# Kernel optimization log

Hardware: AMD Instinct MI355X
Metric: run time of the kernel (lower is better)

Reference implementation:

```python
import jax, jax.numpy as jnp
import numpy as np

BS, TS, NE, ED = 32, 64, 64, 128
AE = 256          # attn_embed_dim
NH = 4            # attn heads
HD = AE // NH     # head dim
RH = 256          # rnn_hidden_dim
NA = 8            # n_agents
NACT = 64         # n_actions
NEG = -1e10


def setup_inputs() -> dict:
    key = jax.random.key(0)
    ks = iter(jax.random.split(key, 64))
    def g(shape, s=0.05):
        return jax.random.normal(next(ks), shape, dtype=jnp.float32) * s
    inp = dict(
        entities=g((BS, TS, NE, ED), 1.0),
        obs_mask=jax.random.randint(next(ks), (BS, TS, NE, NE), 0, 2, dtype=jnp.int32),
        entity_mask=jax.random.randint(next(ks), (BS, TS, NE), 0, 2, dtype=jnp.int32),
        hidden_q=g((BS, NA, RH), 1.0),
        hidden_pi=g((BS, NA, RH), 1.0),
    )
    for p in ('q', 'p'):
        inp[f'{p}_fc1_w'] = g((AE, ED)); inp[f'{p}_fc1_b'] = g((AE,))
        inp[f'{p}_fc2_w'] = g((RH, AE)); inp[f'{p}_fc2_b'] = g((RH,))
        inp[f'{p}_gru_wih'] = g((3 * RH, RH)); inp[f'{p}_gru_whh'] = g((3 * RH, RH))
        inp[f'{p}_gru_bih'] = g((3 * RH,)); inp[f'{p}_gru_bhh'] = g((3 * RH,))
        inp[f'{p}_fcq_w'] = g((NACT, RH)); inp[f'{p}_fcq_b'] = g((NACT,))
        inp[f'{p}_fcpi_w'] = g((NACT, RH)); inp[f'{p}_fcpi_b'] = g((NACT,))
    inp['q_attn_in_w'] = g((3 * AE, AE))
    inp['q_attn_out_w'] = g((AE, AE)); inp['q_attn_out_b'] = g((AE,))
    return inp


def _attention(x1, pre_mask, in_w, out_w, out_b):
    # x1: [B, NE, AE]; pre_mask: [B, NA, NE] (1 = masked)
    qkv = x1 @ in_w.T                                   # [B, NE, 3*AE]
    q, k, v = jnp.split(qkv, 3, axis=-1)
    q = q[:, :NA].reshape(-1, NA, NH, HD).transpose(0, 2, 1, 3)   # [B,H,NA,HD]
    k = k.reshape(-1, NE, NH, HD).transpose(0, 2, 1, 3)           # [B,H,NE,HD]
    v = v.reshape(-1, NE, NH, HD).transpose(0, 2, 1, 3)
    logits = jnp.einsum('bhqd,bhkd->bhqk', q, k) / jnp.sqrt(jnp.float32(HD))
    m = (pre_mask[:, None, :, :] != 0)                  # [B,1,NA,NE]
    dead = jnp.all(m, axis=-1, keepdims=True)           # fully-masked rows -> NaN fix
    logits = jnp.where(m, -jnp.inf, logits)
    logits = jnp.where(dead, 0.0, logits)
    w = jax.nn.softmax(logits, axis=-1)
    w = jnp.where(dead, 0.0, w)                         # torch: masked_fill(NaN, 0)
    out = jnp.einsum('bhqk,bhkd->bhqd', w, v)
    out = out.transpose(0, 2, 1, 3).reshape(-1, NA, AE)
    return out @ out_w.T + out_b


def _gru_scan(x3, h0, wih, whh, bih, bhh):
    # x3: [BS, TS, NA, RH]; h0: [BS*NA, RH]
    xt = x3.transpose(1, 0, 2, 3).reshape(TS, BS * NA, RH)
    def step(h, x):
        gi = x @ wih.T + bih
        gh = h @ whh.T + bhh
        ir, iz, inn = jnp.split(gi, 3, axis=-1)
        hr, hz, hn = jnp.split(gh, 3, axis=-1)
        r = jax.nn.sigmoid(ir + hr)
        z = jax.nn.sigmoid(iz + hz)
        n = jnp.tanh(inn + r * hn)
        h_new = (1.0 - z) * n + z * h
        return h_new, h_new
    _, hs = jax.lax.scan(step, h0, xt)
    return hs.reshape(TS, BS, NA, RH).transpose(1, 0, 2, 3)       # [BS,TS,NA,RH]


def _module(entities, obs_mask, entity_mask, hidden, use_attn,
            fc1_w, fc1_b, fc2_w, fc2_b, gru_wih, gru_whh, gru_bih, gru_bhh,
            fcq_w, fcq_b, fcpi_w, fcpi_b, attn=None):
    B = BS * TS
    e = entities.reshape(B, NE, ED)
    om = obs_mask.reshape(B, NE, NE)
    em = entity_mask.reshape(B, NE)
    agent_mask = em[:, :NA]                              # [B, NA]
    x1 = jax.nn.relu(e @ fc1_w.T + fc1_b)                # [B, NE, AE]
    if use_attn:
        in_w, out_w, out_b = attn
        x2 = _attention(x1, om[:, :NA], in_w, out_w, out_b)
        x2 = jnp.where(agent_mask[:, :, None] != 0, 0.0, x2)   # post_mask
    else:
        x2 = x1[:, :NA]
    x3 = jax.nn.relu(x2 @ fc2_w.T + fc2_b).reshape(BS, TS, NA, RH)
    hs = _gru_scan(x3, hidden.reshape(-1, RH), gru_wih, gru_whh, gru_bih, gru_bhh)
    oq = hs @ fcq_w.T + fcq_b
    opi = hs @ fcpi_w.T + fcpi_b
    am = (agent_mask.reshape(BS, TS, NA, 1) != 0)
    oq = jnp.where(am, 0.0, oq)
    opi = jnp.where(am, NEG, opi)
    return oq, opi, hs


def reference(entities, obs_mask, entity_mask, hidden_q, hidden_pi,
              q_fc1_w, q_fc1_b, q_attn_in_w, q_attn_out_w, q_attn_out_b,
              q_fc2_w, q_fc2_b, q_gru_wih, q_gru_whh, q_gru_bih, q_gru_bhh,
              q_fcq_w, q_fcq_b, q_fcpi_w, q_fcpi_b,
              p_fc1_w, p_fc1_b, p_fc2_w, p_fc2_b,
              p_gru_wih, p_gru_whh, p_gru_bih, p_gru_bhh,
              p_fcq_w, p_fcq_b, p_fcpi_w, p_fcpi_b):
    q, pi, h_q = _module(entities, obs_mask, entity_mask, hidden_q, True,
                         q_fc1_w, q_fc1_b, q_fc2_w, q_fc2_b,
                         q_gru_wih, q_gru_whh, q_gru_bih, q_gru_bhh,
                         q_fcq_w, q_fcq_b, q_fcpi_w, q_fcpi_b,
                         attn=(q_attn_in_w, q_attn_out_w, q_attn_out_b))
    _, pi_avg, h_pi = _module(entities, obs_mask, entity_mask, hidden_pi, False,
                              p_fc1_w, p_fc1_b, p_fc2_w, p_fc2_b,
                              p_gru_wih, p_gru_whh, p_gru_bih, p_gru_bhh,
                              p_fcq_w, p_fcq_b, p_fcpi_w, p_fcpi_b)
    return (q, pi, pi_avg, h_q, h_pi)
```

## Files before the change

### kernel.cpp

```cpp
#include <hip/hip_runtime.h>

typedef unsigned short ushort_t;
typedef __attribute__((ext_vector_type(4))) float f32x4;
typedef __attribute__((ext_vector_type(8))) short s16x8;
typedef __attribute__((ext_vector_type(4))) short s16x4;

#define MFMA16(a, b, c) __builtin_amdgcn_mfma_f32_16x16x32_bf16((a), (b), (c), 0, 0, 0)

__device__ __forceinline__ float us2f(unsigned short u) {
  union { unsigned int i; float f; } v; v.i = ((unsigned int)u) << 16; return v.f;
}
__device__ __forceinline__ unsigned short f2us(float f) {
  union { float f; unsigned int i; } v; v.f = f;
  unsigned int x = v.i;
  return (unsigned short)((x + 0x7FFFu + ((x >> 16) & 1u)) >> 16);
}
__device__ __forceinline__ s16x8 ld8f(const float* p) {
  f32x4 a = *reinterpret_cast<const f32x4*>(p);
  f32x4 b = *reinterpret_cast<const f32x4*>(p + 4);
  s16x8 r;
  r[0] = (short)f2us(a[0]); r[1] = (short)f2us(a[1]);
  r[2] = (short)f2us(a[2]); r[3] = (short)f2us(a[3]);
  r[4] = (short)f2us(b[0]); r[5] = (short)f2us(b[1]);
  r[6] = (short)f2us(b[2]); r[7] = (short)f2us(b[3]);
  return r;
}
__device__ __forceinline__ float sigm(float x) { return 1.0f / (1.0f + __expf(-x)); }
__device__ __forceinline__ float tanh_f(float x) {
  float e = __expf(-2.0f * fabsf(x));
  float t = (1.0f - e) / (1.0f + e);
  return x < 0.0f ? -t : t;
}

__global__ __launch_bounds__(256) void conv_k(
    const float* __restrict__ s0, const float* __restrict__ s1,
    const float* __restrict__ s2, const float* __restrict__ s3,
    ushort_t* __restrict__ d) {
  int i = blockIdx.x * 256 + threadIdx.x;
  if (i >= 155648) return;
  long e = (long)i * 4;
  const float* s; long off;
  if (e < 196608) { s = s0; off = e; }
  else if (e < 393216) { s = s1; off = e - 196608; }
  else if (e < 425984) { s = s2; off = e - 393216; }
  else { s = s3; off = e - 425984; }
  f32x4 v = *reinterpret_cast<const f32x4*>(s + off);
  s16x4 r;
  r[0] = (short)f2us(v[0]); r[1] = (short)f2us(v[1]);
  r[2] = (short)f2us(v[2]); r[3] = (short)f2us(v[3]);
  *reinterpret_cast<s16x4*>(d + e) = r;
}

template <int BN, int EPI, int ROWSEL, int RELU, int AF32, int OF32, int GIT>
__global__ __launch_bounds__(256) void gemm_k(
    const void* __restrict__ A_, const float* __restrict__ W,
    const float* __restrict__ bias, const int* __restrict__ em,
    void* __restrict__ out_, int M, int N, int K) {
  constexpr int NF = (BN == 128) ? 4 : 2;
  const float* Af = (const float*)A_;
  const ushort_t* Ab = (const ushort_t*)A_;
  float* outf = (float*)out_;
  ushort_t* outb = (ushort_t*)out_;
  __shared__ ushort_t As[128 * 40];
  __shared__ ushort_t Ws[BN * 40];
  const int tid = threadIdx.x;
  const int lane = tid & 63;
  const int wid = tid >> 6;
  const int wm = wid & 1, wn = wid >> 1;
  const int m0 = blockIdx.x * 128;
  const int n0 = blockIdx.y * BN;
  const int fr = lane & 15;
  const int kb = (lane >> 4) * 8;

  f32x4 acc[4][NF];
#pragma unroll
  for (int i = 0; i < 4; i++)
#pragma unroll
    for (int j = 0; j < NF; j++) acc[i][j] = (f32x4){0.f, 0.f, 0.f, 0.f};

  for (int k0 = 0; k0 < K; k0 += 32) {
    __syncthreads();
    for (int c = tid; c < 512; c += 256) {
      int row = c >> 2, kc = (c & 3) * 8;
      int gr = m0 + row;
      long ar = ROWSEL ? ((long)(gr >> 3) * 64 + (gr & 7)) : (long)gr;
      s16x8 vv;
      if (AF32) vv = ld8f(&Af[ar * (long)K + k0 + kc]);
      else vv = *reinterpret_cast<const s16x8*>(&Ab[ar * (long)K + k0 + kc]);
      *reinterpret_cast<s16x8*>(&As[row * 40 + kc]) = vv;
    }
    for (int c = tid; c < BN * 4; c += 256) {
      int row = c >> 2, kc = (c & 3) * 8;
      *reinterpret_cast<s16x8*>(&Ws[row * 40 + kc]) =
          ld8f(&W[(long)(n0 + row) * K + k0 + kc]);
    }
    __syncthreads();
    s16x8 af[4], wf[NF];
#pragma unroll
    for (int mi = 0; mi < 4; mi++)
      af[mi] = *reinterpret_cast<const s16x8*>(&As[(wm * 64 + mi * 16 + fr) * 40 + kb]);
#pragma unroll
    for (int ni = 0; ni < NF; ni++)
      wf[ni] = *reinterpret_cast<const s16x8*>(&Ws[(wn * (BN / 2) + ni * 16 + fr) * 40 + kb]);
#pragma unroll
    for (int mi = 0; mi < 4; mi++)
#pragma unroll
      for (int ni = 0; ni < NF; ni++) acc[mi][ni] = MFMA16(af[mi], wf[ni], acc[mi][ni]);
  }

  const int rb = (lane >> 4) * 4;
#pragma unroll
  for (int ni = 0; ni < NF; ni++) {
    int col = n0 + wn * (BN / 2) + ni * 16 + fr;
    float bv = bias[col];
#pragma unroll
    for (int mi = 0; mi < 4; mi++) {
#pragma unroll
      for (int rr = 0; rr < 4; rr++) {
        int row = m0 + wm * 64 + mi * 16 + rb + rr;
        float v = acc[mi][ni][rr] + bv;
        if (RELU) v = fmaxf(v, 0.0f);
        if (EPI == 2 || EPI == 3) {
          if (em[(long)(row >> 3) * 64 + (row & 7)] != 0) v = (EPI == 2) ? 0.0f : -1.0e10f;
        }
        if (GIT) {
          int t = (row >> 3) & 63, bs = row >> 9, na = row & 7;
          int chain = bs * 8 + na;
          int g = col >> 8, cw = col & 255;
          outb[(((long)t * 3 + g) * 16 + (chain >> 4)) * 4096 + cw * 16 + (chain & 15)] =
              f2us(v);
        } else if (OF32) {
          outf[(long)row * N + col] = v;
        } else {
          outb[(long)row * N + col] = f2us(v);
        }
      }
    }
  }
}

__global__ __launch_bounds__(512) void attn_k(
    const float* __restrict__ ent, const int* __restrict__ obs,
    const ushort_t* __restrict__ fc1w, const float* __restrict__ fc1b,
    const ushort_t* __restrict__ inw, ushort_t* __restrict__ attn_out) {
  __shared__ ushort_t x1s[64 * 264];
  __shared__ ushort_t ks[64 * 264];
  __shared__ ushort_t vs[64 * 264];
  __shared__ ushort_t wbuf[256 * 40];
  __shared__ ushort_t es[64 * 136];
  __shared__ float qs[8 * 256];
  __shared__ float lg[32 * 64];
  __shared__ int oms[512];

  const long b = blockIdx.x;
  const int tid = threadIdx.x;
  const int lane = tid & 63, wid = tid >> 6;
  const int mf = wid & 3, nh = wid >> 2;
  const int fr = lane & 15, kb = (lane >> 4) * 8, rb = (lane >> 4) * 4;

  oms[tid] = obs[b * 4096 + tid];
  for (int c = tid; c < 1024; c += 512) {
    int row = c >> 4, kc = (c & 15) * 8;
    *reinterpret_cast<s16x8*>(&es[row * 136 + kc]) =
        ld8f(&ent[b * 8192 + row * 128 + kc]);
  }
  __syncthreads();

  {
    f32x4 a1[8];
#pragma unroll
    for (int i = 0; i < 8; i++) a1[i] = (f32x4){0.f, 0.f, 0.f, 0.f};
    for (int k0 = 0; k0 < 128; k0 += 32) {
      __syncthreads();
      for (int c = tid; c < 1024; c += 512) {
        int row = c >> 2, kc = (c & 3) * 8;
        *reinterpret_cast<s16x8*>(&wbuf[row * 40 + kc]) =
            *reinterpret_cast<const s16x8*>(&fc1w[row * 128 + k0 + kc]);
      }
      __syncthreads();
      s16x8 af = *reinterpret_cast<const s16x8*>(&es[(mf * 16 + fr) * 136 + k0 + kb]);
#pragma unroll
      for (int ni = 0; ni < 8; ni++) {
        s16x8 wf = *reinterpret_cast<const s16x8*>(&wbuf[(nh * 128 + ni * 16 + fr) * 40 + kb]);
        a1[ni] = MFMA16(af, wf, a1[ni]);
      }
    }
#pragma unroll
    for (int ni = 0; ni < 8; ni++) {
      int col = nh * 128 + ni * 16 + fr;
      float bv = fc1b[col];
#pragma unroll
      for (int rr = 0; rr < 4; rr++) {
        int row = mf * 16 + rb + rr;
        x1s[row * 264 + col] = f2us(fmaxf(a1[ni][rr] + bv, 0.0f));
      }
    }
  }
  {
    f32x4 a2[8];
#pragma unroll
    for (int i = 0; i < 8; i++) a2[i] = (f32x4){0.f, 0.f, 0.f, 0.f};
    for (int k0 = 0; k0 < 256; k0 += 32) {
      __syncthreads();
      for (int c = tid; c < 1024; c += 512) {
        int row = c >> 2, kc = (c & 3) * 8;
        *reinterpret_cast<s16x8*>(&wbuf[row * 40 + kc]) =
            *reinterpret_cast<const s16x8*>(&inw[65536 + row * 256 + k0 + kc]);
      }
      __syncthreads();
      s16x8 af = *reinterpret_cast<const s16x8*>(&x1s[(mf * 16 + fr) * 264 + k0 + kb]);
#pragma unroll
      for (int ni = 0; ni < 8; ni++) {
        s16x8 wf = *reinterpret_cast<const s16x8*>(&wbuf[(nh * 128 + ni * 16 + fr) * 40 + kb]);
        a2[ni] = MFMA16(af, wf, a2[ni]);
      }
    }
#pragma unroll
    for (int ni = 0; ni < 8; ni++) {
      int col = nh * 128 + ni * 16 + fr;
#pragma unroll
      for (int rr = 0; rr < 4; rr++) ks[(mf * 16 + rb + rr) * 264 + col] = f2us(a2[ni][rr]);
    }
  }
  {
    f32x4 a3[8];
#pragma unroll
    for (int i = 0; i < 8; i++) a3[i] = (f32x4){0.f, 0.f, 0.f, 0.f};
    for (int k0 = 0; k0 < 256; k0 += 32) {
      __syncthreads();
      for (int c = tid; c < 1024; c += 512) {
        int row = c >> 2, kc = (c & 3) * 8;
        *reinterpret_cast<s16x8*>(&wbuf[row * 40 + kc]) =
            *reinterpret_cast<const s16x8*>(&inw[131072 + row * 256 + k0 + kc]);
      }
      __syncthreads();
      s16x8 af = *reinterpret_cast<const s16x8*>(&x1s[(mf * 16 + fr) * 264 + k0 + kb]);
#pragma unroll
      for (int ni = 0; ni < 8; ni++) {
        s16x8 wf = *reinterpret_cast<const s16x8*>(&wbuf[(nh * 128 + ni * 16 + fr) * 40 + kb]);
        a3[ni] = MFMA16(af, wf, a3[ni]);
      }
    }
#pragma unroll
    for (int ni = 0; ni < 8; ni++) {
      int col = nh * 128 + ni * 16 + fr;
#pragma unroll
      for (int rr = 0; rr < 4; rr++) vs[(mf * 16 + rb + rr) * 264 + col] = f2us(a3[ni][rr]);
    }
  }
  {
    f32x4 aq[2];
    aq[0] = (f32x4){0.f, 0.f, 0.f, 0.f};
    aq[1] = (f32x4){0.f, 0.f, 0.f, 0.f};
    for (int k0 = 0; k0 < 256; k0 += 32) {
      __syncthreads();
      for (int c = tid; c < 1024; c += 512) {
        int row = c >> 2, kc = (c & 3) * 8;
        *reinterpret_cast<s16x8*>(&wbuf[row * 40 + kc]) =
            *reinterpret_cast<const s16x8*>(&inw[row * 256 + k0 + kc]);
      }
      __syncthreads();
      s16x8 af = *reinterpret_cast<const s16x8*>(&x1s[fr * 264 + k0 + kb]);
#pragma unroll
      for (int i = 0; i < 2; i++) {
        int nf2 = wid * 2 + i;
        s16x8 wf = *reinterpret_cast<const s16x8*>(&wbuf[(nf2 * 16 + fr) * 40 + kb]);
        aq[i] = MFMA16(af, wf, aq[i]);
      }
    }
#pragma unroll
    for (int i = 0; i < 2; i++) {
#pragma unroll
      for (int rr = 0; rr < 4; rr++) {
        int row = rb + rr;
        if (row < 8) qs[row * 256 + (wid * 2 + i) * 16 + fr] = aq[i][rr] * 0.125f;
      }
    }
  }
  __syncthreads();

  for (int i = 0; i < 4; i++) {
    int idx = tid + 512 * i;
    int a = idx >> 8, h = (idx >> 6) & 3, e = idx & 63;
    const float* qrow = &qs[a * 256 + h * 64];
    const ushort_t* krow = &ks[e * 264 + h * 64];
    float s = 0.0f;
    for (int d = 0; d < 64; d++) s += qrow[d] * us2f(krow[d]);
    lg[(a * 4 + h) * 64 + e] = (oms[a * 64 + e] != 0) ? -1.0e30f : s;
  }
  __syncthreads();
  if (tid < 32) {
    int a = tid >> 2;
    float* row = &lg[tid * 64];
    bool dead = true;
    for (int e = 0; e < 64; e++)
      if (oms[a * 64 + e] == 0) { dead = false; break; }
    if (dead) {
      for (int e = 0; e < 64; e++) row[e] = 0.0f;
    } else {
      float mx = -1.0e30f;
      for (int e = 0; e < 64; e++) mx = fmaxf(mx, row[e]);
      float sum = 0.0f;
      for (int e = 0; e < 64; e++) { float ex = __expf(row[e] - mx); row[e] = ex; sum += ex; }
      float inv = 1.0f / sum;
      for (int e = 0; e < 64; e++) row[e] *= inv;
    }
  }
  __syncthreads();
  for (int i = 0; i < 4; i++) {
    int idx = tid + 512 * i;
    int a = idx >> 8, d = idx & 255, h = d >> 6;
    const float* wrow = &lg[(a * 4 + h) * 64];
    float s = 0.0f;
    for (int e = 0; e < 64; e++) s += wrow[e] * us2f(vs[e * 264 + d]);
    attn_out[((long)b * 8 + a) * 256 + d] = f2us(s);
  }
}

__global__ __launch_bounds__(1024) void gru3_k(
    const ushort_t* __restrict__ giT_q, const ushort_t* __restrict__ giT_p,
    const ushort_t* __restrict__ whhb_q, const ushort_t* __restrict__ whhb_p,
    const float* __restrict__ bhh_q, const float* __restrict__ bhh_p,
    const float* __restrict__ h0_q, const float* __restrict__ h0_p,
    float* __restrict__ hs_q, float* __restrict__ hs_p) {
  __shared__ ushort_t nw[256 * 256];
  __shared__ ushort_t hls[16 * 260];
  const int bid = blockIdx.x;
  const int mdl = bid >> 4, cg = bid & 15;
  const ushort_t* giT = mdl ? giT_p : giT_q;
  const ushort_t* whh = mdl ? whhb_p : whhb_q;
  const float* bhh = mdl ? bhh_p : bhh_q;
  const float* h0 = mdl ? h0_p : h0_q;
  float* hs = mdl ? hs_p : hs_q;

  const int tid = threadIdx.x;
  const int lane = tid & 63, w = tid >> 6;
  const int fr = lane & 15, kb = (lane >> 4) * 8, rb = (lane >> 4) * 4;
  const int c0 = w * 16;
  const int col = c0 + fr;

  s16x8 wrz[2][8];
#pragma unroll
  for (int g = 0; g < 2; g++)
#pragma unroll
    for (int ks = 0; ks < 8; ks++)
      wrz[g][ks] = *reinterpret_cast<const s16x8*>(
          &whh[(g * 256 + col) * 256 + ks * 32 + kb]);

  char* nwb = (char*)nw;
  for (int c = tid; c < 8192; c += 1024) {
    int row = c >> 5, kc = (c & 31) * 8;
    *reinterpret_cast<s16x8*>(nwb + row * 512 + ((kc * 2) ^ ((row & 7) << 4))) =
        *reinterpret_cast<const s16x8*>(&whh[(512 + row) * 256 + kc]);
  }

  float h[4], bh[3];
#pragma unroll
  for (int rr = 0; rr < 4; rr++) h[rr] = h0[(cg * 16 + rb + rr) * 256 + col];
#pragma unroll
  for (int g = 0; g < 3; g++) bh[g] = bhh[g * 256 + col];

  long hsb[4];
#pragma unroll
  for (int rr = 0; rr < 4; rr++) {
    int chain = cg * 16 + rb + rr;
    hsb[rr] = ((long)((chain >> 3) * 64) * 8 + (chain & 7)) * 256 + col;
  }

  for (int t = 0; t < 64; t++) {
    s16x4 gv[3];
#pragma unroll
    for (int g = 0; g < 3; g++)
      gv[g] = *reinterpret_cast<const s16x4*>(
          &giT[(((long)t * 3 + g) * 16 + cg) * 4096 + col * 16 + rb]);
#pragma unroll
    for (int rr = 0; rr < 4; rr++) hls[(rb + rr) * 260 + col] = f2us(h[rr]);
    __syncthreads();
    f32x4 acc[3];
#pragma unroll
    for (int i = 0; i < 3; i++) acc[i] = (f32x4){0.f, 0.f, 0.f, 0.f};
#pragma unroll
    for (int ks = 0; ks < 8; ks++) {
      s16x8 a = *reinterpret_cast<const s16x8*>(&hls[fr * 260 + ks * 32 + kb]);
      acc[0] = MFMA16(a, wrz[0][ks], acc[0]);
      acc[1] = MFMA16(a, wrz[1][ks], acc[1]);
      s16x8 bn = *reinterpret_cast<const s16x8*>(
          nwb + col * 512 + (((ks * 32 + kb) * 2) ^ ((col & 7) << 4)));
      acc[2] = MFMA16(a, bn, acc[2]);
    }
    __syncthreads();
#pragma unroll
    for (int rr = 0; rr < 4; rr++) {
      float r_ = sigm(us2f((unsigned short)gv[0][rr]) + acc[0][rr] + bh[0]);
      float z_ = sigm(us2f((unsigned short)gv[1][rr]) + acc[1][rr] + bh[1]);
      float n_ = tanh_f(us2f((unsigned short)gv[2][rr]) + r_ * (acc[2][rr] + bh[2]));
      float hn = (1.0f - z_) * n_ + z_ * h[rr];
      h[rr] = hn;
      hs[hsb[rr] + (long)t * 2048] = hn;
    }
  }
}

extern "C" void kernel_launch(void* const* d_in, const int* in_sizes, int n_in,
                              void* d_out, int out_size, void* d_ws, size_t ws_size,
                              hipStream_t stream) {
  (void)in_sizes; (void)n_in; (void)out_size; (void)ws_size;

  const float* entities = (const float*)d_in[0];
  const int* obs = (const int*)d_in[1];
  const int* em = (const int*)d_in[2];
  const float* hidq = (const float*)d_in[3];
  const float* hidp = (const float*)d_in[4];
  const float* q_fc1_w = (const float*)d_in[5];
  const float* q_fc1_b = (const float*)d_in[6];
  const float* q_fc2_w = (const float*)d_in[7];
  const float* q_fc2_b = (const float*)d_in[8];
  const float* q_wih = (const float*)d_in[9];
  const float* q_whh = (const float*)d_in[10];
  const float* q_bih = (const float*)d_in[11];
  const float* q_bhh = (const float*)d_in[12];
  const float* q_fcq_w = (const float*)d_in[13];
  const float* q_fcq_b = (const float*)d_in[14];
  const float* q_fcpi_w = (const float*)d_in[15];
  const float* q_fcpi_b = (const float*)d_in[16];
  const float* p_fc1_w = (const float*)d_in[17];
  const float* p_fc1_b = (const float*)d_in[18];
  const float* p_fc2_w = (const float*)d_in[19];
  const float* p_fc2_b = (const float*)d_in[20];
  const float* p_wih = (const float*)d_in[21];
  const float* p_whh = (const float*)d_in[22];
  const float* p_bih = (const float*)d_in[23];
  const float* p_bhh = (const float*)d_in[24];
  const float* p_fcpi_w = (const float*)d_in[27];
  const float* p_fcpi_b = (const float*)d_in[28];
  const float* inw = (const float*)d_in[29];
  const float* outw = (const float*)d_in[30];
  const float* outb = (const float*)d_in[31];

  ushort_t* ws = (ushort_t*)d_ws;
  ushort_t* R0 = ws;
  ushort_t* R1 = ws + 4194304l;
  ushort_t* giq = ws + 8388608l;
  ushort_t* gip = ws + 20971520l;
  ushort_t* wcv = ws + 33554432l;
  ushort_t* wbq = wcv;
  ushort_t* wbp = wcv + 196608l;
  ushort_t* wf1 = wcv + 393216l;
  ushort_t* win = wcv + 425984l;

  float* out = (float*)d_out;
  float* o_q = out;
  float* o_pi = out + 1048576l;
  float* o_piA = out + 2097152l;
  float* o_hq = out + 3145728l;
  float* o_hp = out + 7340032l;

  conv_k<<<608, 256, 0, stream>>>(q_whh, p_whh, q_fc1_w, inw, wcv);
  attn_k<<<2048, 512, 0, stream>>>(entities, obs, wf1, q_fc1_b, win, R0);
  gemm_k<128, 2, 0, 0, 0, 0, 0><<<dim3(128, 2), 256, 0, stream>>>(R0, outw, outb, em, R1, 16384, 256, 256);
  gemm_k<128, 0, 0, 1, 0, 0, 0><<<dim3(128, 2), 256, 0, stream>>>(R1, q_fc2_w, q_fc2_b, em, R0, 16384, 256, 256);
  gemm_k<128, 0, 0, 0, 0, 0, 1><<<dim3(128, 6), 256, 0, stream>>>(R0, q_wih, q_bih, em, giq, 16384, 768, 256);
  gemm_k<128, 0, 1, 1, 1, 0, 0><<<dim3(128, 2), 256, 0, stream>>>(entities, p_fc1_w, p_fc1_b, em, R1, 16384, 256, 128);
  gemm_k<128, 0, 0, 1, 0, 0, 0><<<dim3(128, 2), 256, 0, stream>>>(R1, p_fc2_w, p_fc2_b, em, R0, 16384, 256, 256);
  gemm_k<128, 0, 0, 0, 0, 0, 1><<<dim3(128, 6), 256, 0, stream>>>(R0, p_wih, p_bih, em, gip, 16384, 768, 256);
  gru3_k<<<32, 1024, 0, stream>>>(giq, gip, wbq, wbp, q_bhh, p_bhh, hidq, hidp,
                                  o_hq, o_hp);
  gemm_k<64, 2, 0, 0, 1, 1, 0><<<dim3(128, 1), 256, 0, stream>>>(o_hq, q_fcq_w, q_fcq_b, em, o_q, 16384, 64, 256);
  gemm_k<64, 3, 0, 0, 1, 1, 0><<<dim3(128, 1), 256, 0, stream>>>(o_hq, q_fcpi_w, q_fcpi_b, em, o_pi, 16384, 64, 256);
  gemm_k<64, 3, 0, 0, 1, 1, 0><<<dim3(128, 1), 256, 0, stream>>>(o_hp, p_fcpi_w, p_fcpi_b, em, o_piA, 16384, 64, 256);
}
```

Before: 556.9 us.

## Split attention into batched fc1/QKV GEMMs plus MFMA-based attention kernel

The monolithic per-batch attention kernel, which recomputed fc1 and the Q/K/V projections with weights streamed through shared memory for every block, is replaced by large tiled GEMMs for fc1 and the fused QKV projection, followed by a lighter attention kernel. That kernel computes logits with MFMA, runs a parallel shuffle-based softmax and vectorises the weighted V sum. Work is chunked by workspace size, and the weight conversion kernel shrinks. It adds intermediate global traffic for x1 and K/V, plus chunked launches when the workspace is small.

After: 714.6 us. 28.3% more time.

```diff
diff --git a/kernel.cpp b/kernel.cpp
--- a/kernel.cpp
+++ b/kernel.cpp
@@ -34,16 +34,13 @@
 
 __global__ __launch_bounds__(256) void conv_k(
     const float* __restrict__ s0, const float* __restrict__ s1,
-    const float* __restrict__ s2, const float* __restrict__ s3,
     ushort_t* __restrict__ d) {
   int i = blockIdx.x * 256 + threadIdx.x;
-  if (i >= 155648) return;
+  if (i >= 98304) return;
   long e = (long)i * 4;
   const float* s; long off;
   if (e < 196608) { s = s0; off = e; }
-  else if (e < 393216) { s = s1; off = e - 196608; }
-  else if (e < 425984) { s = s2; off = e - 393216; }
-  else { s = s3; off = e - 425984; }
+  else { s = s1; off = e - 196608; }
   f32x4 v = *reinterpret_cast<const f32x4*>(s + off);
   s16x4 r;
   r[0] = (short)f2us(v[0]); r[1] = (short)f2us(v[1]);
@@ -51,11 +48,13 @@
   *reinterpret_cast<s16x4*>(d + e) = r;
 }
 
-template <int BN, int EPI, int ROWSEL, int RELU, int AF32, int OF32, int GIT>
+template <int BN, int EPI, int ROWSEL, int RELU, int AF32, int OF32, int GIT,
+          int QKV, int HB>
 __global__ __launch_bounds__(256) void gemm_k(
     const void* __restrict__ A_, const float* __restrict__ W,
     const float* __restrict__ bias, const int* __restrict__ em,
-    void* __restrict__ out_, int M, int N, int K) {
+    void* __restrict__ out_, ushort_t* __restrict__ qout, long row0,
+    int M, int N, int K) {
   constexpr int NF = (BN == 128) ? 4 : 2;
   const float* Af = (const float*)A_;
   const ushort_t* Ab = (const ushort_t*)A_;
@@ -112,7 +111,7 @@
 #pragma unroll
   for (int ni = 0; ni < NF; ni++) {
     int col = n0 + wn * (BN / 2) + ni * 16 + fr;
-    float bv = bias[col];
+    float bv = HB ? bias[col] : 0.0f;
 #pragma unroll
     for (int mi = 0; mi < 4; mi++) {
 #pragma unroll
@@ -123,7 +122,15 @@
         if (EPI == 2 || EPI == 3) {
           if (em[(long)(row >> 3) * 64 + (row & 7)] != 0) v = (EPI == 2) ? 0.0f : -1.0e10f;
         }
-        if (GIT) {
+        if (QKV) {
+          long grow = row0 + row;
+          int e = (int)(grow & 63);
+          if (col < 256) {
+            if (e < 8) qout[((grow >> 6) * 8 + e) * 256 + col] = f2us(v * 0.125f);
+          } else {
+            outb[(long)row * 512 + (col - 256)] = f2us(v);
+          }
+        } else if (GIT) {
           int t = (row >> 3) & 63, bs = row >> 9, na = row & 7;
           int chain = bs * 8 + na;
           int g = col >> 8, cw = col & 255;
@@ -139,181 +146,105 @@
   }
 }
 
-__global__ __launch_bounds__(512) void attn_k(
-    const float* __restrict__ ent, const int* __restrict__ obs,
-    const ushort_t* __restrict__ fc1w, const float* __restrict__ fc1b,
-    const ushort_t* __restrict__ inw, ushort_t* __restrict__ attn_out) {
-  __shared__ ushort_t x1s[64 * 264];
+__global__ __launch_bounds__(512) void attn2_k(
+    const ushort_t* __restrict__ kv, const ushort_t* __restrict__ qbuf,
+    const int* __restrict__ obs, ushort_t* __restrict__ attn_out, int b0) {
+  __shared__ ushort_t qs[16 * 264];
   __shared__ ushort_t ks[64 * 264];
   __shared__ ushort_t vs[64 * 264];
-  __shared__ ushort_t wbuf[256 * 40];
-  __shared__ ushort_t es[64 * 136];
-  __shared__ float qs[8 * 256];
-  __shared__ float lg[32 * 64];
+  __shared__ float lg[32 * 66];
   __shared__ int oms[512];
 
-  const long b = blockIdx.x;
+  const int b_loc = blockIdx.x;
+  const long b = b0 + b_loc;
   const int tid = threadIdx.x;
-  const int lane = tid & 63, wid = tid >> 6;
-  const int mf = wid & 3, nh = wid >> 2;
+  const int lane = tid & 63;
+  const int w = tid >> 6;
   const int fr = lane & 15, kb = (lane >> 4) * 8, rb = (lane >> 4) * 4;
 
   oms[tid] = obs[b * 4096 + tid];
-  for (int c = tid; c < 1024; c += 512) {
-    int row = c >> 4, kc = (c & 15) * 8;
-    *reinterpret_cast<s16x8*>(&es[row * 136 + kc]) =
-        ld8f(&ent[b * 8192 + row * 128 + kc]);
+  {
+    int row = tid >> 5, cc = (tid & 31) * 8;
+    if (tid < 256) {
+      *reinterpret_cast<s16x8*>(&qs[row * 264 + cc]) =
+          *reinterpret_cast<const s16x8*>(&qbuf[(b * 8 + row) * 256 + cc]);
+    } else {
+      *reinterpret_cast<s16x8*>(&qs[row * 264 + cc]) = (s16x8){0,0,0,0,0,0,0,0};
+    }
+  }
+  for (int i = 0; i < 4; i++) {
+    int e = i * 16 + (tid >> 5);
+    int cc = (tid & 31) * 8;
+    const ushort_t* src = &kv[((long)(b_loc * 64 + e)) * 512];
+    *reinterpret_cast<s16x8*>(&ks[e * 264 + cc]) =
+        *reinterpret_cast<const s16x8*>(&src[cc]);
+    *reinterpret_cast<s16x8*>(&vs[e * 264 + cc]) =
+        *reinterpret_cast<const s16x8*>(&src[256 + cc]);
   }
   __syncthreads();
 
   {
-    f32x4 a1[8];
-#pragma unroll
-    for (int i = 0; i < 8; i++) a1[i] = (f32x4){0.f, 0.f, 0.f, 0.f};
-    for (int k0 = 0; k0 < 128; k0 += 32) {
-      __syncthreads();
-      for (int c = tid; c < 1024; c += 512) {
-        int row = c >> 2, kc = (c & 3) * 8;
-        *reinterpret_cast<s16x8*>(&wbuf[row * 40 + kc]) =
-            *reinterpret_cast<const s16x8*>(&fc1w[row * 128 + k0 + kc]);
+    const int h = w >> 1, np = w & 1;
+    f32x4 lacc[2];
+    lacc[0] = (f32x4){0.f, 0.f, 0.f, 0.f};
+    lacc[1] = (f32x4){0.f, 0.f, 0.f, 0.f};
+#pragma unroll
+    for (int k0 = 0; k0 < 64; k0 += 32) {
+      s16x8 af = *reinterpret_cast<const s16x8*>(&qs[fr * 264 + h * 64 + k0 + kb]);
+#pragma unroll
+      for (int j = 0; j < 2; j++) {
+        int e0 = (np * 2 + j) * 16;
+        s16x8 bf = *reinterpret_cast<const s16x8*>(&ks[(e0 + fr) * 264 + h * 64 + k0 + kb]);
+        lacc[j] = MFMA16(af, bf, lacc[j]);
       }
-      __syncthreads();
-      s16x8 af = *reinterpret_cast<const s16x8*>(&es[(mf * 16 + fr) * 136 + k0 + kb]);
-#pragma unroll
-      for (int ni = 0; ni < 8; ni++) {
-        s16x8 wf = *reinterpret_cast<const s16x8*>(&wbuf[(nh * 128 + ni * 16 + fr) * 40 + kb]);
-        a1[ni] = MFMA16(af, wf, a1[ni]);
+    }
+#pragma unroll
+    for (int j = 0; j < 2; j++) {
+      int e = (np * 2 + j) * 16 + fr;
+#pragma unroll
+      for (int rr = 0; rr < 4; rr++) {
+        int a = rb + rr;
+        if (a < 8)
+          lg[(a * 4 + h) * 66 + e] = (oms[a * 64 + e] != 0) ? -1.0e30f : lacc[j][rr];
       }
     }
-#pragma unroll
-    for (int ni = 0; ni < 8; ni++) {
-      int col = nh * 128 + ni * 16 + fr;
-      float bv = fc1b[col];
-#pragma unroll
-      for (int rr = 0; rr < 4; rr++) {
-        int row = mf * 16 + rb + rr;
-        x1s[row * 264 + col] = f2us(fmaxf(a1[ni][rr] + bv, 0.0f));
-      }
-    }
-  }
+  }
+  __syncthreads();
+
   {
-    f32x4 a2[8];
-#pragma unroll
-    for (int i = 0; i < 8; i++) a2[i] = (f32x4){0.f, 0.f, 0.f, 0.f};
-    for (int k0 = 0; k0 < 256; k0 += 32) {
-      __syncthreads();
-      for (int c = tid; c < 1024; c += 512) {
-        int row = c >> 2, kc = (c & 3) * 8;
-        *reinterpret_cast<s16x8*>(&wbuf[row * 40 + kc]) =
-            *reinterpret_cast<const s16x8*>(&inw[65536 + row * 256 + k0 + kc]);
-      }
-      __syncthreads();
-      s16x8 af = *reinterpret_cast<const s16x8*>(&x1s[(mf * 16 + fr) * 264 + k0 + kb]);
-#pragma unroll
-      for (int ni = 0; ni < 8; ni++) {
-        s16x8 wf = *reinterpret_cast<const s16x8*>(&wbuf[(nh * 128 + ni * 16 + fr) * 40 + kb]);
-        a2[ni] = MFMA16(af, wf, a2[ni]);
-      }
-    }
-#pragma unroll
-    for (int ni = 0; ni < 8; ni++) {
-      int col = nh * 128 + ni * 16 + fr;
-#pragma unroll
-      for (int rr = 0; rr < 4; rr++) ks[(mf * 16 + rb + rr) * 264 + col] = f2us(a2[ni][rr]);
-    }
-  }
+    int ri = tid >> 4, sub = tid & 15;
+    float v4[4];
+#pragma unroll
+    for (int j = 0; j < 4; j++) v4[j] = lg[ri * 66 + sub * 4 + j];
+    float m = fmaxf(fmaxf(v4[0], v4[1]), fmaxf(v4[2], v4[3]));
+#pragma unroll
+    for (int d = 1; d < 16; d <<= 1) m = fmaxf(m, __shfl_xor(m, d));
+    bool dead = (m < -5.0e29f);
+    float s = 0.0f;
+#pragma unroll
+    for (int j = 0; j < 4; j++) { v4[j] = __expf(v4[j] - m); s += v4[j]; }
+#pragma unroll
+    for (int d = 1; d < 16; d <<= 1) s += __shfl_xor(s, d);
+    float inv = dead ? 0.0f : (1.0f / s);
+#pragma unroll
+    for (int j = 0; j < 4; j++) lg[ri * 66 + sub * 4 + j] = v4[j] * inv;
+  }
+  __syncthreads();
+
   {
-    f32x4 a3[8];
-#pragma unroll
-    for (int i = 0; i < 8; i++) a3[i] = (f32x4){0.f, 0.f, 0.f, 0.f};
-    for (int k0 = 0; k0 < 256; k0 += 32) {
-      __syncthreads();
-      for (int c = tid; c < 1024; c += 512) {
-        int row = c >> 2, kc = (c & 3) * 8;
-        *reinterpret_cast<s16x8*>(&wbuf[row * 40 + kc]) =
-            *reinterpret_cast<const s16x8*>(&inw[131072 + row * 256 + k0 + kc]);
-      }
-      __syncthreads();
-      s16x8 af = *reinterpret_cast<const s16x8*>(&x1s[(mf * 16 + fr) * 264 + k0 + kb]);
-#pragma unroll
-      for (int ni = 0; ni < 8; ni++) {
-        s16x8 wf = *reinterpret_cast<const s16x8*>(&wbuf[(nh * 128 + ni * 16 + fr) * 40 + kb]);
-        a3[ni] = MFMA16(af, wf, a3[ni]);
-      }
-    }
-#pragma unroll
-    for (int ni = 0; ni < 8; ni++) {
-      int col = nh * 128 + ni * 16 + fr;
-#pragma unroll
-      for (int rr = 0; rr < 4; rr++) vs[(mf * 16 + rb + rr) * 264 + col] = f2us(a3[ni][rr]);
-    }
-  }
-  {
-    f32x4 aq[2];
-    aq[0] = (f32x4){0.f, 0.f, 0.f, 0.f};
-    aq[1] = (f32x4){0.f, 0.f, 0.f, 0.f};
-    for (int k0 = 0; k0 < 256; k0 += 32) {
-      __syncthreads();
-      for (int c = tid; c < 1024; c += 512) {
-        int row = c >> 2, kc = (c & 3) * 8;
-        *reinterpret_cast<s16x8*>(&wbuf[row * 40 + kc]) =
-            *reinterpret_cast<const s16x8*>(&inw[row * 256 + k0 + kc]);
-      }
-      __syncthreads();
-      s16x8 af = *reinterpret_cast<const s16x8*>(&x1s[fr * 264 + k0 + kb]);
-#pragma unroll
-      for (int i = 0; i < 2; i++) {
-        int nf2 = wid * 2 + i;
-        s16x8 wf = *reinterpret_cast<const s16x8*>(&wbuf[(nf2 * 16 + fr) * 40 + kb]);
-        aq[i] = MFMA16(af, wf, aq[i]);
-      }
-    }
-#pragma unroll
-    for (int i = 0; i < 2; i++) {
-#pragma unroll
-      for (int rr = 0; rr < 4; rr++) {
-        int row = rb + rr;
-        if (row < 8) qs[row * 256 + (wid * 2 + i) * 16 + fr] = aq[i][rr] * 0.125f;
-      }
-    }
-  }
-  __syncthreads();
-
-  for (int i = 0; i < 4; i++) {
-    int idx = tid + 512 * i;
-    int a = idx >> 8, h = (idx >> 6) & 3, e = idx & 63;
-    const float* qrow = &qs[a * 256 + h * 64];
-    const ushort_t* krow = &ks[e * 264 + h * 64];
-    float s = 0.0f;
-    for (int d = 0; d < 64; d++) s += qrow[d] * us2f(krow[d]);
-    lg[(a * 4 + h) * 64 + e] = (oms[a * 64 + e] != 0) ? -1.0e30f : s;
-  }
-  __syncthreads();
-  if (tid < 32) {
-    int a = tid >> 2;
-    float* row = &lg[tid * 64];
-    bool dead = true;
-    for (int e = 0; e < 64; e++)
-      if (oms[a * 64 + e] == 0) { dead = false; break; }
-    if (dead) {
-      for (int e = 0; e < 64; e++) row[e] = 0.0f;
-    } else {
-      float mx = -1.0e30f;
-      for (int e = 0; e < 64; e++) mx = fmaxf(mx, row[e]);
-      float sum = 0.0f;
-      for (int e = 0; e < 64; e++) { float ex = __expf(row[e] - mx); row[e] = ex; sum += ex; }
-      float inv = 1.0f / sum;
-      for (int e = 0; e < 64; e++) row[e] *= inv;
-    }
-  }
-  __syncthreads();
-  for (int i = 0; i < 4; i++) {
-    int idx = tid + 512 * i;
-    int a = idx >> 8, d = idx & 255, h = d >> 6;
-    const float* wrow = &lg[(a * 4 + h) * 64];
-    float s = 0.0f;
-    for (int e = 0; e < 64; e++) s += wrow[e] * us2f(vs[e * 264 + d]);
-    attn_out[((long)b * 8 + a) * 256 + d] = f2us(s);
+    int a = tid >> 6, d0 = (tid & 63) * 4, h = d0 >> 6;
+    const float* wrow = &lg[(a * 4 + h) * 66];
+    float facc[4] = {0.f, 0.f, 0.f, 0.f};
+    for (int e = 0; e < 64; e++) {
+      float wv = wrow[e];
+      s16x4 vv = *reinterpret_cast<const s16x4*>(&vs[e * 264 + d0]);
+#pragma unroll
+      for (int j = 0; j < 4; j++) facc[j] += wv * us2f((unsigned short)vv[j]);
+    }
+    s16x4 r;
+#pragma unroll
+    for (int j = 0; j < 4; j++) r[j] = (short)f2us(facc[j]);
+    *reinterpret_cast<s16x4*>(&attn_out[(b * 8 + a) * 256 + d0]) = r;
   }
 }
 
@@ -336,8 +267,7 @@
   const int tid = threadIdx.x;
   const int lane = tid & 63, w = tid >> 6;
   const int fr = lane & 15, kb = (lane >> 4) * 8, rb = (lane >> 4) * 4;
-  const int c0 = w * 16;
-  const int col = c0 + fr;
+  const int col = w * 16 + fr;
 
   s16x8 wrz[2][8];
 #pragma unroll
@@ -404,7 +334,7 @@
 extern "C" void kernel_launch(void* const* d_in, const int* in_sizes, int n_in,
                               void* d_out, int out_size, void* d_ws, size_t ws_size,
                               hipStream_t stream) {
-  (void)in_sizes; (void)n_in; (void)out_size; (void)ws_size;
+  (void)in_sizes; (void)n_in; (void)out_size;
 
   const float* entities = (const float*)d_in[0];
   const int* obs = (const int*)d_in[1];
@@ -438,15 +368,24 @@
   const float* outb = (const float*)d_in[31];
 
   ushort_t* ws = (ushort_t*)d_ws;
-  ushort_t* R0 = ws;
-  ushort_t* R1 = ws + 4194304l;
-  ushort_t* giq = ws + 8388608l;
-  ushort_t* gip = ws + 20971520l;
-  ushort_t* wcv = ws + 33554432l;
+  const int big = (ws_size >= (size_t)218890240) ? 1 : 0;
+  const int nc = big ? 1 : 4;
+  const int CB = 2048 / nc;
+  const long MR = (long)CB * 64;
+
+  ushort_t* qbuf = ws;
+  ushort_t* attn = ws + 4194304l;
+  ushort_t* x1c = ws + 8388608l;
+  ushort_t* kvc = big ? (ws + 41943040l) : (ws + 16777216l);
+  ushort_t* wcv = big ? (ws + 109051904l) : (ws + 33554432l);
   ushort_t* wbq = wcv;
   ushort_t* wbp = wcv + 196608l;
-  ushort_t* wf1 = wcv + 393216l;
-  ushort_t* win = wcv + 425984l;
+  ushort_t* x2b = ws + 8388608l;
+  ushort_t* x3q = ws + 20971520l;
+  ushort_t* giq = ws + 8388608l;
+  ushort_t* x1p = ws + 4194304l;
+  ushort_t* x3p = ws;
+  ushort_t* gip = ws + 20971520l;
 
   float* out = (float*)d_out;
   float* o_q = out;
@@ -455,17 +394,34 @@
   float* o_hq = out + 3145728l;
   float* o_hp = out + 7340032l;
 
-  conv_k<<<608, 256, 0, stream>>>(q_whh, p_whh, q_fc1_w, inw, wcv);
-  attn_k<<<2048, 512, 0, stream>>>(entities, obs, wf1, q_fc1_b, win, R0);
-  gemm_k<128, 2, 0, 0, 0, 0, 0><<<dim3(128, 2), 256, 0, stream>>>(R0, outw, outb, em, R1, 16384, 256, 256);
-  gemm_k<128, 0, 0, 1, 0, 0, 0><<<dim3(128, 2), 256, 0, stream>>>(R1, q_fc2_w, q_fc2_b, em, R0, 16384, 256, 256);
-  gemm_k<128, 0, 0, 0, 0, 0, 1><<<dim3(128, 6), 256, 0, stream>>>(R0, q_wih, q_bih, em, giq, 16384, 768, 256);
-  gemm_k<128, 0, 1, 1, 1, 0, 0><<<dim3(128, 2), 256, 0, stream>>>(entities, p_fc1_w, p_fc1_b, em, R1, 16384, 256, 128);
-  gemm_k<128, 0, 0, 1, 0, 0, 0><<<dim3(128, 2), 256, 0, stream>>>(R1, p_fc2_w, p_fc2_b, em, R0, 16384, 256, 256);
-  gemm_k<128, 0, 0, 0, 0, 0, 1><<<dim3(128, 6), 256, 0, stream>>>(R0, p_wih, p_bih, em, gip, 16384, 768, 256);
+  conv_k<<<384, 256, 0, stream>>>(q_whh, p_whh, wcv);
+
+  for (int c = 0; c < nc; c++) {
+    gemm_k<128, 0, 0, 1, 1, 0, 0, 0, 1><<<dim3(MR / 128, 2), 256, 0, stream>>>(
+        entities + (long)c * MR * 128, q_fc1_w, q_fc1_b, em, x1c, nullptr, 0,
+        (int)MR, 256, 128);
+    gemm_k<128, 0, 0, 0, 0, 0, 0, 1, 0><<<dim3(MR / 128, 6), 256, 0, stream>>>(
+        x1c, inw, q_fc1_b, em, kvc, qbuf, (long)c * MR, (int)MR, 768, 256);
+    attn2_k<<<CB, 512, 0, stream>>>(kvc, qbuf, obs, attn, c * CB);
+  }
+  gemm_k<128, 2, 0, 0, 0, 0, 0, 0, 1><<<dim3(128, 2), 256, 0, stream>>>(
+      attn, outw, outb, em, x2b, nullptr, 0, 16384, 256, 256);
+  gemm_k<128, 0, 0, 1, 0, 0, 0, 0, 1><<<dim3(128, 2), 256, 0, stream>>>(
+      x2b, q_fc2_w, q_fc2_b, em, x3q, nullptr, 0, 16384, 256, 256);
+  gemm_k<128, 0, 0, 0, 0, 0, 1, 0, 1><<<dim3(128, 6), 256, 0, stream>>>(
+      x3q, q_wih, q_bih, em, giq, nullptr, 0, 16384, 768, 256);
+  gemm_k<128, 0, 1, 1, 1, 0, 0, 0, 1><<<dim3(128, 2), 256, 0, stream>>>(
+      entities, p_fc1_w, p_fc1_b, em, x1p, nullptr, 0, 16384, 256, 128);
+  gemm_k<128, 0, 0, 1, 0, 0, 0, 0, 1><<<dim3(128, 2), 256, 0, stream>>>(
+      x1p, p_fc2_w, p_fc2_b, em, x3p, nullptr, 0, 16384, 256, 256);
+  gemm_k<128, 0, 0, 0, 0, 0, 1, 0, 1><<<dim3(128, 6), 256, 0, stream>>>(
+      x3p, p_wih, p_bih, em, gip, nullptr, 0, 16384, 768, 256);
   gru3_k<<<32, 1024, 0, stream>>>(giq, gip, wbq, wbp, q_bhh, p_bhh, hidq, hidp,
                                   o_hq, o_hp);
-  gemm_k<64, 2, 0, 0, 1, 1, 0><<<dim3(128, 1), 256, 0, stream>>>(o_hq, q_fcq_w, q_fcq_b, em, o_q, 16384, 64, 256);
-  gemm_k<64, 3, 0, 0, 1, 1, 0><<<dim3(128, 1), 256, 0, stream>>>(o_hq, q_fcpi_w, q_fcpi_b, em, o_pi, 16384, 64, 256);
-  gemm_k<64, 3, 0, 0, 1, 1, 0><<<dim3(128, 1), 256, 0, stream>>>(o_hp, p_fcpi_w, p_fcpi_b, em, o_piA, 16384, 64, 256);
-}
+  gemm_k<64, 2, 0, 0, 1, 1, 0, 0, 1><<<dim3(128, 1), 256, 0, stream>>>(
+      o_hq, q_fcq_w, q_fcq_b, em, o_q, nullptr, 0, 16384, 64, 256);
+  gemm_k<64, 3, 0, 0, 1, 1, 0, 0, 1><<<dim3(128, 1), 256, 0, stream>>>(
+      o_hq, q_fcpi_w, q_fcpi_b, em, o_pi, nullptr, 0, 16384, 64, 256);
+  gemm_k<64, 3, 0, 0, 1, 1, 0, 0, 1><<<dim3(128, 1), 256, 0, stream>>>(
+      o_hp, p_fcpi_w, p_fcpi_b, em, o_piA, nullptr, 0, 16384, 64, 256);
+}
```
